# Optimization experiments

Hardware: AMD Instinct MI355X
Metric: run time of the kernel (lower is better)

The kernel has to match this reference:

```python
import jax, jax.numpy as jnp
import numpy as np

N_NODES = 50000
N_GROUPS = 512
D_FEAT = 128
D_HID = 128
N_CLASS = 16
NEG_SLOPE = 0.2


def gat_conv(x, edge_index, W, a_src, a_dst, bias, n):
    """Single-head PyG-style GATConv (with self-loops, eval mode / no dropout)."""
    h = x @ W  # [n, D_HID]
    loop = jnp.arange(n)
    src = jnp.concatenate([edge_index[0], loop])  # neighbors j
    dst = jnp.concatenate([edge_index[1], loop])  # targets i
    a_s = h @ a_src  # [n]
    a_d = h @ a_dst  # [n]
    e = jax.nn.leaky_relu(a_s[src] + a_d[dst], NEG_SLOPE)  # [E+n]
    # segment softmax over incoming edges of each dst node
    m = jax.ops.segment_max(e, dst, num_segments=n)
    e = jnp.exp(e - m[dst])
    denom = jax.ops.segment_sum(e, dst, num_segments=n)
    alpha = e / denom[dst]
    out = jax.ops.segment_sum(alpha[:, None] * h[src], dst, num_segments=n)
    return out + bias


def setup_inputs() -> dict:
    key = jax.random.key(0)
    ks = jax.random.split(key, 12)
    s_f = 1.0 / np.sqrt(D_FEAT)
    s_h = 1.0 / np.sqrt(D_HID)
    return {
        "x_full": jax.random.normal(ks[0], (N_NODES, D_FEAT), jnp.float32),
        "x_group": jax.random.normal(ks[1], (N_GROUPS, D_FEAT), jnp.float32),
        "W_full": jax.random.normal(ks[2], (D_FEAT, D_HID), jnp.float32) * s_f,
        "a_src_full": jax.random.normal(ks[3], (D_HID,), jnp.float32) * s_h,
        "a_dst_full": jax.random.normal(ks[4], (D_HID,), jnp.float32) * s_h,
        "bias_full": jnp.zeros((D_HID,), jnp.float32),
        "W_group": jax.random.normal(ks[5], (D_FEAT, D_HID), jnp.float32) * s_f,
        "a_src_group": jax.random.normal(ks[6], (D_HID,), jnp.float32) * s_h,
        "a_dst_group": jax.random.normal(ks[7], (D_HID,), jnp.float32) * s_h,
        "bias_group": jnp.zeros((D_HID,), jnp.float32),
        "fc_W": jax.random.normal(ks[8], (D_HID, N_CLASS), jnp.float32) * s_h,
        "fc_b": jnp.zeros((N_CLASS,), jnp.float32),
        "edge_index_full": jax.random.randint(ks[9], (2, 600000), 0, N_NODES, jnp.int64),
        "edge_index_group": jax.random.randint(ks[10], (2, 4096), 0, N_GROUPS, jnp.int64),
        "node_group": jax.random.randint(ks[11], (N_NODES,), 0, N_GROUPS, jnp.int64),
    }


def reference(x_full, x_group, W_full, a_src_full, a_dst_full, bias_full,
              W_group, a_src_group, a_dst_group, bias_group, fc_W, fc_b,
              edge_index_full, edge_index_group, node_group):
    full_x = jax.nn.elu(gat_conv(x_full, edge_index_full, W_full, a_src_full,
                                 a_dst_full, bias_full, N_NODES))   # [N, D_HID]
    group_x = jax.nn.elu(gat_conv(x_group, edge_index_group, W_group, a_src_group,
                                  a_dst_group, bias_group, N_GROUPS))  # [G, D_HID]

    # mean feature of groups adjacent to each group (edges src->dst in group graph)
    gsrc, gdst = edge_index_group[0], edge_index_group[1]
    adj_sum = jax.ops.segment_sum(group_x[gdst], gsrc, num_segments=N_GROUPS)
    cnt = jax.ops.segment_sum(jnp.ones_like(gsrc, jnp.float32), gsrc, num_segments=N_GROUPS)
    adj_mean = adj_sum / jnp.maximum(cnt, 1.0)[:, None]  # [G, D_HID]

    gf = group_x[node_group]   # group feature per node, [N, D_HID]
    am = adj_mean[node_group]  # adjacent-group mean per node, [N, D_HID]

    # dot(node, group_feature) and mean_j dot(node, adj_j) == dot(node, adj_mean)
    iw_group = jnp.sum(full_x * gf, axis=-1, keepdims=True)  # [N, 1]
    iw_adj = jnp.sum(full_x * am, axis=-1, keepdims=True)    # [N, 1]

    updated = full_x + iw_group * gf + iw_adj * am  # [N, D_HID]
    out = updated @ fc_W + fc_b                     # [N, N_CLASS]
    return (out, updated)
```

## Files before the change

kernel.cpp:

```cpp
#include <hip/hip_runtime.h>

typedef unsigned short u16;
typedef unsigned int u32;

static __device__ __forceinline__ float lrelu(float x) { return x >= 0.f ? x : 0.2f * x; }

static __device__ __forceinline__ u16 f2bf(float f) {
    u32 u = __float_as_uint(f);
    u += 0x7FFF + ((u >> 16) & 1);
    return (u16)(u >> 16);
}
static __device__ __forceinline__ float bf2f(u16 h) {
    return __uint_as_float((u32)h << 16);
}

static __device__ __forceinline__ float fc_reduce16(float f0, float f1, int lane,
                                                    const float4* __restrict__ fW4) {
    float4 w00 = fW4[(2 * lane) * 4 + 0], w01 = fW4[(2 * lane) * 4 + 1];
    float4 w02 = fW4[(2 * lane) * 4 + 2], w03 = fW4[(2 * lane) * 4 + 3];
    float4 w10 = fW4[(2 * lane + 1) * 4 + 0], w11 = fW4[(2 * lane + 1) * 4 + 1];
    float4 w12 = fW4[(2 * lane + 1) * 4 + 2], w13 = fW4[(2 * lane + 1) * 4 + 3];
    float4 q0, q1, q2, q3;
    q0.x = f0 * w00.x + f1 * w10.x; q0.y = f0 * w00.y + f1 * w10.y;
    q0.z = f0 * w00.z + f1 * w10.z; q0.w = f0 * w00.w + f1 * w10.w;
    q1.x = f0 * w01.x + f1 * w11.x; q1.y = f0 * w01.y + f1 * w11.y;
    q1.z = f0 * w01.z + f1 * w11.z; q1.w = f0 * w01.w + f1 * w11.w;
    q2.x = f0 * w02.x + f1 * w12.x; q2.y = f0 * w02.y + f1 * w12.y;
    q2.z = f0 * w02.z + f1 * w12.z; q2.w = f0 * w02.w + f1 * w12.w;
    q3.x = f0 * w03.x + f1 * w13.x; q3.y = f0 * w03.y + f1 * w13.y;
    q3.z = f0 * w03.z + f1 * w13.z; q3.w = f0 * w03.w + f1 * w13.w;
    bool h5 = (lane & 32) != 0, h4 = (lane & 16) != 0;
    bool h3 = (lane & 8) != 0, h2 = (lane & 4) != 0;
    float4 s0, s1, k0, k1;
    s0.x = h5 ? q0.x : q2.x; s0.y = h5 ? q0.y : q2.y;
    s0.z = h5 ? q0.z : q2.z; s0.w = h5 ? q0.w : q2.w;
    s1.x = h5 ? q1.x : q3.x; s1.y = h5 ? q1.y : q3.y;
    s1.z = h5 ? q1.z : q3.z; s1.w = h5 ? q1.w : q3.w;
    s0.x = __shfl_xor(s0.x, 32); s0.y = __shfl_xor(s0.y, 32);
    s0.z = __shfl_xor(s0.z, 32); s0.w = __shfl_xor(s0.w, 32);
    s1.x = __shfl_xor(s1.x, 32); s1.y = __shfl_xor(s1.y, 32);
    s1.z = __shfl_xor(s1.z, 32); s1.w = __shfl_xor(s1.w, 32);
    k0.x = h5 ? q2.x : q0.x; k0.y = h5 ? q2.y : q0.y;
    k0.z = h5 ? q2.z : q0.z; k0.w = h5 ? q2.w : q0.w;
    k1.x = h5 ? q3.x : q1.x; k1.y = h5 ? q3.y : q1.y;
    k1.z = h5 ? q3.z : q1.z; k1.w = h5 ? q3.w : q1.w;
    float4 a0, a1;
    a0.x = k0.x + s0.x; a0.y = k0.y + s0.y; a0.z = k0.z + s0.z; a0.w = k0.w + s0.w;
    a1.x = k1.x + s1.x; a1.y = k1.y + s1.y; a1.z = k1.z + s1.z; a1.w = k1.w + s1.w;
    float4 sB, kB;
    sB.x = h4 ? a0.x : a1.x; sB.y = h4 ? a0.y : a1.y;
    sB.z = h4 ? a0.z : a1.z; sB.w = h4 ? a0.w : a1.w;
    sB.x = __shfl_xor(sB.x, 16); sB.y = __shfl_xor(sB.y, 16);
    sB.z = __shfl_xor(sB.z, 16); sB.w = __shfl_xor(sB.w, 16);
    kB.x = h4 ? a1.x : a0.x; kB.y = h4 ? a1.y : a0.y;
    kB.z = h4 ? a1.z : a0.z; kB.w = h4 ? a1.w : a0.w;
    float4 b;
    b.x = kB.x + sB.x; b.y = kB.y + sB.y; b.z = kB.z + sB.z; b.w = kB.w + sB.w;
    float sCx = h3 ? b.x : b.z, sCy = h3 ? b.y : b.w;
    sCx = __shfl_xor(sCx, 8); sCy = __shfl_xor(sCy, 8);
    float kCx = h3 ? b.z : b.x, kCy = h3 ? b.w : b.y;
    float c2x = kCx + sCx, c2y = kCy + sCy;
    float sD = h2 ? c2x : c2y;
    sD = __shfl_xor(sD, 4);
    float kD = h2 ? c2y : c2x;
    float r = kD + sD;
    r += __shfl_xor(r, 1);
    r += __shfl_xor(r, 2);
    return r;
}

__global__ __launch_bounds__(256) void gemm_both_kernel(
        const float* __restrict__ Xf, const float* __restrict__ Wf,
        const float* __restrict__ asf, const float* __restrict__ adf,
        u16* __restrict__ Hbf, float* __restrict__ as_f, float* __restrict__ ad_f, int N,
        const float* __restrict__ Xg, const float* __restrict__ Wg,
        const float* __restrict__ asg, const float* __restrict__ adg,
        u16* __restrict__ Hbg, float* __restrict__ as_g, float* __restrict__ ad_g, int G,
        int nbFull) {
    const float* X; const float* W; const float* av; const float* dv;
    u16* Hb; float* as_out; float* ad_out; int n_lim; long base;
    if (blockIdx.x < nbFull) {
        X = Xf; W = Wf; av = asf; dv = adf; Hb = Hbf; as_out = as_f; ad_out = ad_f;
        n_lim = N; base = (long)blockIdx.x * 32;
    } else {
        X = Xg; W = Wg; av = asg; dv = adg; Hb = Hbg; as_out = as_g; ad_out = ad_g;
        n_lim = G; base = (long)(blockIdx.x - nbFull) * 32;
    }
    __shared__ float Ws[64 * 128];
    __shared__ float Xs[32 * 128];
    int tid = threadIdx.x;
    float4* Ws4 = (float4*)Ws;
    float4* Xs4 = (float4*)Xs;
    const float4* X4 = (const float4*)(X + base * 128);
    for (int i = tid; i < 1024; i += 256) {
        int r = i >> 5;
        Xs4[i] = (base + r < n_lim) ? X4[i] : make_float4(0.f, 0.f, 0.f, 0.f);
    }
    int fgrp = tid & 31;
    int n0 = (tid >> 5) * 4;
    float4 acc[4] = {};
    for (int half = 0; half < 2; ++half) {
        __syncthreads();
        const float4* W4 = (const float4*)(W + half * 64 * 128);
        for (int i = tid; i < 2048; i += 256) Ws4[i] = W4[i];
        __syncthreads();
        #pragma unroll 4
        for (int kk = 0; kk < 64; ++kk) {
            float4 w = Ws4[kk * 32 + fgrp];
            #pragma unroll
            for (int j = 0; j < 4; ++j) {
                float x = Xs[(n0 + j) * 128 + half * 64 + kk];
                acc[j].x += x * w.x; acc[j].y += x * w.y;
                acc[j].z += x * w.z; acc[j].w += x * w.w;
            }
        }
    }
    float4 as4 = ((const float4*)av)[fgrp];
    float4 ad4 = ((const float4*)dv)[fgrp];
    float ps[4], pd[4];
    #pragma unroll
    for (int j = 0; j < 4; ++j) {
        ps[j] = acc[j].x * as4.x + acc[j].y * as4.y + acc[j].z * as4.z + acc[j].w * as4.w;
        pd[j] = acc[j].x * ad4.x + acc[j].y * ad4.y + acc[j].z * ad4.z + acc[j].w * ad4.w;
    }
    #pragma unroll
    for (int off = 16; off; off >>= 1) {
        #pragma unroll
        for (int j = 0; j < 4; ++j) {
            ps[j] += __shfl_xor(ps[j], off);
            pd[j] += __shfl_xor(pd[j], off);
        }
    }
    if ((tid & 31) == 0) {
        #pragma unroll
        for (int j = 0; j < 4; ++j) {
            long n = base + n0 + j;
            if (n < n_lim) { as_out[n] = ps[j]; ad_out[n] = pd[j]; }
        }
    }
    #pragma unroll
    for (int j = 0; j < 4; ++j) {
        long n = base + n0 + j;
        if (n < n_lim) {
            ushort4 hv;
            hv.x = f2bf(acc[j].x); hv.y = f2bf(acc[j].y);
            hv.z = f2bf(acc[j].z); hv.w = f2bf(acc[j].w);
            ((ushort4*)(Hb + n * 128))[fgrp] = hv;
        }
    }
}

__global__ __launch_bounds__(256) void hist2_kernel(const int* __restrict__ efd, int E, int N,
                                                    const int* __restrict__ egd, int Eg, int G,
                                                    int Npad, int* __restrict__ deg) {
    int i = blockIdx.x * 256 + threadIdx.x;
    int totF = E + N;
    int tot = totF + Eg + G;
    if (i >= tot) return;
    int d;
    if (i < E) d = efd[i];
    else if (i < totF) d = i - E;
    else {
        int j = i - totF;
        d = Npad + ((j < Eg) ? egd[j] : (j - Eg));
    }
    atomicAdd(&deg[d], 1);
}

__global__ __launch_bounds__(256) void scan1_kernel(const int* __restrict__ deg, int n,
                                                    int* __restrict__ bsum) {
    __shared__ int s[256];
    int i = blockIdx.x * 256 + threadIdx.x;
    s[threadIdx.x] = (i < n) ? deg[i] : 0;
    __syncthreads();
    for (int off = 128; off; off >>= 1) {
        if (threadIdx.x < off) s[threadIdx.x] += s[threadIdx.x + off];
        __syncthreads();
    }
    if (threadIdx.x == 0) bsum[blockIdx.x] = s[0];
}

__global__ __launch_bounds__(256) void scan3_kernel(int* __restrict__ deg, int n, int nb,
                                                    const int* __restrict__ bsum,
                                                    int* __restrict__ offs, int Ltot) {
    __shared__ int sb[256];
    __shared__ int s[256];
    int t = threadIdx.x;
    sb[t] = (t < nb) ? bsum[t] : 0;
    __syncthreads();
    for (int off = 1; off < 256; off <<= 1) {
        int u = (t >= off) ? sb[t - off] : 0;
        __syncthreads();
        sb[t] += u;
        __syncthreads();
    }
    int blockOff = (blockIdx.x == 0) ? 0 : sb[blockIdx.x - 1];
    if (blockIdx.x == 0 && t == 0) offs[Ltot] = sb[nb - 1];

    int i = blockIdx.x * 256 + t;
    int v = (i < n) ? deg[i] : 0;
    s[t] = v;
    __syncthreads();
    for (int off = 1; off < 256; off <<= 1) {
        int u = (t >= off) ? s[t - off] : 0;
        __syncthreads();
        s[t] += u;
        __syncthreads();
    }
    if (i < n) {
        int excl = s[t] - v + blockOff;
        offs[i] = excl;
        deg[i] = excl;
    }
}

__global__ __launch_bounds__(256) void place2_kernel(const int* __restrict__ efs,
                                                     const int* __restrict__ efd, int E, int N,
                                                     const int* __restrict__ egs,
                                                     const int* __restrict__ egd, int Eg, int G,
                                                     int Npad,
                                                     const float* __restrict__ a_s,
                                                     const float* __restrict__ a_d,
                                                     const float* __restrict__ a_sg,
                                                     const float* __restrict__ a_dg,
                                                     int* __restrict__ cursor,
                                                     int2* __restrict__ sepack) {
    int i = blockIdx.x * 256 + threadIdx.x;
    int totF = E + N;
    int tot = totF + Eg + G;
    if (i >= tot) return;
    int s, d, dcur;
    float av;
    if (i < totF) {
        if (i < E) { s = efs[i]; d = efd[i]; } else { s = d = i - E; }
        av = a_s[s] + a_d[d];
        dcur = d;
    } else {
        int j = i - totF;
        if (j < Eg) { s = egs[j]; d = egd[j]; } else { s = d = j - Eg; }
        av = a_sg[s] + a_dg[d];
        dcur = Npad + d;
    }
    float e = expf(lrelu(av));
    int pos = atomicAdd(&cursor[dcur], 1);
    sepack[pos] = make_int2(s, __float_as_int(e));
}

__global__ __launch_bounds__(256) void pull2_kernel(const u16* __restrict__ Hf,
                                                    const u16* __restrict__ Hg,
                                                    const int* __restrict__ offs,
                                                    const int2* __restrict__ sepack,
                                                    const float* __restrict__ bias_f,
                                                    const float* __restrict__ bias_g,
                                                    const float* __restrict__ fcW,
                                                    float* __restrict__ fx,
                                                    float* __restrict__ gx,
                                                    float* __restrict__ fxW,
                                                    int N, int G, int Npad) {
    int gid = blockIdx.x * 256 + threadIdx.x;
    int w = gid >> 6, lane = gid & 63;
    const u16* H;
    const float* bias;
    float* out;
    int idx;
    bool isFull = (w < N);
    if (isFull) {
        H = Hf; bias = bias_f; out = fx + (long)w * 128; idx = w;
    } else if (w < N + G) {
        int g = w - N;
        H = Hg; bias = bias_g; out = gx + (long)g * 128; idx = Npad + g;
    } else return;
    int beg = offs[idx], end = offs[idx + 1];
    const ushort2* H2 = (const ushort2*)H;
    float a0x = 0.f, a0y = 0.f, a1x = 0.f, a1y = 0.f;
    float a2x = 0.f, a2y = 0.f, a3x = 0.f, a3y = 0.f;
    float ss0 = 0.f, ss1 = 0.f;
    for (int b = beg; b < end; b += 64) {
        int m = end - b;
        if (m > 64) m = 64;
        int2 se = (lane < m) ? sepack[b + lane] : make_int2(0, 0);
        int sl = se.x;
        float el = __int_as_float(se.y);
        int k = 0;
        for (; k + 4 <= m; k += 4) {
            int s0 = __shfl(sl, k),     s1 = __shfl(sl, k + 1);
            int s2 = __shfl(sl, k + 2), s3 = __shfl(sl, k + 3);
            float e0 = __shfl(el, k),     e1 = __shfl(el, k + 1);
            float e2 = __shfl(el, k + 2), e3 = __shfl(el, k + 3);
            ushort2 h0 = H2[(long)s0 * 64 + lane];
            ushort2 h1 = H2[(long)s1 * 64 + lane];
            ushort2 h2 = H2[(long)s2 * 64 + lane];
            ushort2 h3 = H2[(long)s3 * 64 + lane];
            a0x += e0 * bf2f(h0.x); a0y += e0 * bf2f(h0.y);
            a1x += e1 * bf2f(h1.x); a1y += e1 * bf2f(h1.y);
            a2x += e2 * bf2f(h2.x); a2y += e2 * bf2f(h2.y);
            a3x += e3 * bf2f(h3.x); a3y += e3 * bf2f(h3.y);
            ss0 += e0 + e1; ss1 += e2 + e3;
        }
        for (; k < m; ++k) {
            int s0 = __shfl(sl, k);
            float e0 = __shfl(el, k);
            ushort2 h0 = H2[(long)s0 * 64 + lane];
            a0x += e0 * bf2f(h0.x); a0y += e0 * bf2f(h0.y);
            ss0 += e0;
        }
    }
    float accx = (a0x + a1x) + (a2x + a3x);
    float accy = (a0y + a1y) + (a2y + a3y);
    float ssum = ss0 + ss1;
    float inv = 1.f / ssum;
    float2 bv = ((const float2*)bias)[lane];
    float ox = accx * inv + bv.x;
    float oy = accy * inv + bv.y;
    ox = ox > 0.f ? ox : expm1f(ox);
    oy = oy > 0.f ? oy : expm1f(oy);
    ((float2*)out)[lane] = make_float2(ox, oy);
    if (isFull) {
        float r = fc_reduce16(ox, oy, lane, (const float4*)fcW);
        int cls = (lane >> 2) & 15;
        if ((lane & 3) == 0) fxW[(long)w * 16 + cls] = r;
    }
}

__global__ __launch_bounds__(256) void adj_kernel(const int* __restrict__ gsrc,
                                                  const int* __restrict__ gdst, int Eg,
                                                  const float* __restrict__ gx,
                                                  float* __restrict__ adj_sum,
                                                  float* __restrict__ cnt) {
    int gid = blockIdx.x * 256 + threadIdx.x;
    int i = gid >> 6, lane = gid & 63;
    if (i >= Eg) return;
    int s = gsrc[i], d = gdst[i];
    float2 gv = ((const float2*)gx)[(long)d * 64 + lane];
    atomicAdd(&adj_sum[(long)s * 128 + 2 * lane], gv.x);
    atomicAdd(&adj_sum[(long)s * 128 + 2 * lane + 1], gv.y);
    if (lane == 0) atomicAdd(&cnt[s], 1.f);
}

__global__ __launch_bounds__(256) void groupfc_kernel(const float* __restrict__ gx,
                                                      const float* __restrict__ adj_sum,
                                                      const float* __restrict__ cnt,
                                                      const float* __restrict__ fcW,
                                                      float* __restrict__ adj_mean,
                                                      float* __restrict__ gfW,
                                                      float* __restrict__ amW, int G) {
    int gid = blockIdx.x * 256 + threadIdx.x;
    int g = gid >> 6, lane = gid & 63;
    if (g >= G) return;
    float inv = 1.f / fmaxf(cnt[g], 1.f);
    float2 as2 = ((const float2*)adj_sum)[(long)g * 64 + lane];
    float2 am = make_float2(as2.x * inv, as2.y * inv);
    ((float2*)adj_mean)[(long)g * 64 + lane] = am;
    float2 gf = ((const float2*)gx)[(long)g * 64 + lane];
    const float4* fW4 = (const float4*)fcW;
    float rg = fc_reduce16(gf.x, gf.y, lane, fW4);
    float ra = fc_reduce16(am.x, am.y, lane, fW4);
    int cls = (lane >> 2) & 15;
    if ((lane & 3) == 0) {
        gfW[(long)g * 16 + cls] = rg;
        amW[(long)g * 16 + cls] = ra;
    }
}

__global__ __launch_bounds__(256) void final3_kernel(const int* __restrict__ node_group,
                                                     const float* __restrict__ gx,
                                                     const float* __restrict__ adj_mean,
                                                     const float* __restrict__ gfW,
                                                     const float* __restrict__ amW,
                                                     const float* __restrict__ fxW,
                                                     const float* __restrict__ fcb,
                                                     float* __restrict__ upd,
                                                     float* __restrict__ out, int N) {
    int gid = blockIdx.x * 256 + threadIdx.x;
    int n = gid >> 6, lane = gid & 63;
    if (n >= N) return;
    int g = node_group[n];
    float2 row = ((const float2*)upd)[(long)n * 64 + lane];
    float2 gf = ((const float2*)gx)[(long)g * 64 + lane];
    float2 am = ((const float2*)adj_mean)[(long)g * 64 + lane];
    float pg = row.x * gf.x + row.y * gf.y;
    float pa = row.x * am.x + row.y * am.y;
    #pragma unroll
    for (int off = 32; off; off >>= 1) {
        pg += __shfl_xor(pg, off);
        pa += __shfl_xor(pa, off);
    }
    float ux = row.x + pg * gf.x + pa * am.x;
    float uy = row.y + pg * gf.y + pa * am.y;
    ((float2*)upd)[(long)n * 64 + lane] = make_float2(ux, uy);
    if (lane < 16) {
        out[(long)n * 16 + lane] = fxW[(long)n * 16 + lane] + pg * gfW[(long)g * 16 + lane] +
                                   pa * amW[(long)g * 16 + lane] + fcb[lane];
    }
}

extern "C" void kernel_launch(void* const* d_in, const int* in_sizes, int n_in,
                              void* d_out, int out_size, void* d_ws, size_t ws_size,
                              hipStream_t stream) {
    const float* x_full = (const float*)d_in[0];
    const float* x_group = (const float*)d_in[1];
    const float* W_full = (const float*)d_in[2];
    const float* a_src_full = (const float*)d_in[3];
    const float* a_dst_full = (const float*)d_in[4];
    const float* bias_full = (const float*)d_in[5];
    const float* W_group = (const float*)d_in[6];
    const float* a_src_g = (const float*)d_in[7];
    const float* a_dst_g = (const float*)d_in[8];
    const float* bias_g = (const float*)d_in[9];
    const float* fc_W = (const float*)d_in[10];
    const float* fc_b = (const float*)d_in[11];
    const int* ef = (const int*)d_in[12];
    const int* eg = (const int*)d_in[13];
    const int* node_group = (const int*)d_in[14];

    int N = in_sizes[0] / 128;
    int G = in_sizes[1] / 128;
    int E = in_sizes[12] / 2;
    int Eg = in_sizes[13] / 2;
    const int* ef_src = ef;
    const int* ef_dst = ef + E;
    const int* eg_src = eg;
    const int* eg_dst = eg + Eg;

    int Npad = (N + 255) & ~255;
    int Ltot = Npad + G;
    int LtotPad = (Ltot + 255) & ~255;
    int totF = E + N;
    int tot = totF + Eg + G;

    float* out_cls = (float*)d_out;
    float* fx = out_cls + (long)N * 16;

    char* w = (char*)d_ws;
    auto alloc = [&](size_t bytes) {
        char* p = w;
        w += (bytes + 255) & ~(size_t)255;
        return p;
    };
    u16* h_full = (u16*)alloc((size_t)N * 128 * 2);
    u16* h_g = (u16*)alloc((size_t)G * 128 * 2);
    float* a_s = (float*)alloc((size_t)N * 4);
    float* a_d = (float*)alloc((size_t)N * 4);
    float* a_sg = (float*)alloc((size_t)G * 4);
    float* a_dg = (float*)alloc((size_t)G * 4);
    float* gx = (float*)alloc((size_t)G * 128 * 4);
    float* adj_mean = (float*)alloc((size_t)G * 128 * 4);
    float* fxW = (float*)alloc((size_t)N * 16 * 4);
    float* gfW = (float*)alloc((size_t)G * 16 * 4);
    float* amW = (float*)alloc((size_t)G * 16 * 4);
    float* adj_sum = (float*)alloc((size_t)G * 128 * 4);
    float* cnt = (float*)alloc((size_t)G * 4);
    int* deg = (int*)alloc((size_t)LtotPad * 4);
    int* offs = (int*)alloc((size_t)(LtotPad + 1) * 4);
    int2* sepack = (int2*)alloc((size_t)tot * 8);
    int* bsum = (int*)alloc(256 * 4);

    size_t zero_span = (char*)(deg + LtotPad) - (char*)adj_sum;
    (void)hipMemsetAsync(adj_sum, 0, zero_span, stream);

    auto cdiv = [](int a, int b) { return (a + b - 1) / b; };

    int nbFull = cdiv(N, 32);
    gemm_both_kernel<<<nbFull + cdiv(G, 32), 256, 0, stream>>>(
        x_full, W_full, a_src_full, a_dst_full, h_full, a_s, a_d, N,
        x_group, W_group, a_src_g, a_dst_g, h_g, a_sg, a_dg, G, nbFull);

    int nb = cdiv(Ltot, 256);
    hist2_kernel<<<cdiv(tot, 256), 256, 0, stream>>>(ef_dst, E, N, eg_dst, Eg, G, Npad, deg);
    scan1_kernel<<<nb, 256, 0, stream>>>(deg, Ltot, bsum);
    scan3_kernel<<<nb, 256, 0, stream>>>(deg, Ltot, nb, bsum, offs, Ltot);
    place2_kernel<<<cdiv(tot, 256), 256, 0, stream>>>(ef_src, ef_dst, E, N, eg_src, eg_dst,
                                                      Eg, G, Npad, a_s, a_d, a_sg, a_dg,
                                                      deg, sepack);

    pull2_kernel<<<cdiv((N + G) * 64, 256), 256, 0, stream>>>(h_full, h_g, offs, sepack,
                                                              bias_full, bias_g, fc_W,
                                                              fx, gx, fxW, N, G, Npad);

    adj_kernel<<<cdiv(Eg * 64, 256), 256, 0, stream>>>(eg_src, eg_dst, Eg, gx, adj_sum, cnt);
    groupfc_kernel<<<cdiv(G * 64, 256), 256, 0, stream>>>(gx, adj_sum, cnt, fc_W,
                                                          adj_mean, gfW, amW, G);
    final3_kernel<<<cdiv(N * 64, 256), 256, 0, stream>>>(node_group, gx, adj_mean, gfW, amW,
                                                         fxW, fc_b, fx, out_cls, N);
}
```

Baseline: 289.1 us.

## Pull 4 edges per wave with 16B bf16 loads and move FC into final kernel

The pull kernel now splits each wave into four 16-lane groups. Each group loads a full 256-byte bf16 row with uint4 loads, so the wave processes four source edges per step instead of one, and a cross-group shuffle reduction combines the partial sums. The FC projection is removed from the pull kernel and the group-fc kernel is deleted. The final kernel now computes the adjacent-group mean inline and applies the FC to the updated row directly. The aim is fewer, wider gather loads, one less launch, and fewer intermediate buffers, at the cost of extra shuffle reductions, tail lanes doing padded work, and only 16 lanes active for the epilogue.

```diff
diff --git a/kernel.cpp b/kernel.cpp
--- a/kernel.cpp
+++ b/kernel.cpp
@@ -10,9 +10,8 @@
     u += 0x7FFF + ((u >> 16) & 1);
     return (u16)(u >> 16);
 }
-static __device__ __forceinline__ float bf2f(u16 h) {
-    return __uint_as_float((u32)h << 16);
-}
+static __device__ __forceinline__ float bflo(u32 u) { return __uint_as_float(u << 16); }
+static __device__ __forceinline__ float bfhi(u32 u) { return __uint_as_float(u & 0xffff0000u); }
 
 static __device__ __forceinline__ float fc_reduce16(float f0, float f1, int lane,
                                                     const float4* __restrict__ fW4) {
@@ -252,10 +251,8 @@
                                                     const int2* __restrict__ sepack,
                                                     const float* __restrict__ bias_f,
                                                     const float* __restrict__ bias_g,
-                                                    const float* __restrict__ fcW,
                                                     float* __restrict__ fx,
                                                     float* __restrict__ gx,
-                                                    float* __restrict__ fxW,
                                                     int N, int G, int Npad) {
     int gid = blockIdx.x * 256 + threadIdx.x;
     int w = gid >> 6, lane = gid & 63;
@@ -263,62 +260,84 @@
     const float* bias;
     float* out;
     int idx;
-    bool isFull = (w < N);
-    if (isFull) {
+    if (w < N) {
         H = Hf; bias = bias_f; out = fx + (long)w * 128; idx = w;
     } else if (w < N + G) {
         int g = w - N;
         H = Hg; bias = bias_g; out = gx + (long)g * 128; idx = Npad + g;
     } else return;
     int beg = offs[idx], end = offs[idx + 1];
-    const ushort2* H2 = (const ushort2*)H;
-    float a0x = 0.f, a0y = 0.f, a1x = 0.f, a1y = 0.f;
-    float a2x = 0.f, a2y = 0.f, a3x = 0.f, a3y = 0.f;
-    float ss0 = 0.f, ss1 = 0.f;
+    const uint4* H16 = (const uint4*)H;
+    int sub = lane >> 4;
+    int fc = lane & 15;
+    float a0 = 0.f, a1 = 0.f, a2 = 0.f, a3 = 0.f;
+    float a4 = 0.f, a5 = 0.f, a6 = 0.f, a7 = 0.f;
+    float ss = 0.f;
     for (int b = beg; b < end; b += 64) {
         int m = end - b;
         if (m > 64) m = 64;
         int2 se = (lane < m) ? sepack[b + lane] : make_int2(0, 0);
         int sl = se.x;
         float el = __int_as_float(se.y);
+        int kend = (m + 3) & ~3;
         int k = 0;
-        for (; k + 4 <= m; k += 4) {
-            int s0 = __shfl(sl, k),     s1 = __shfl(sl, k + 1);
-            int s2 = __shfl(sl, k + 2), s3 = __shfl(sl, k + 3);
-            float e0 = __shfl(el, k),     e1 = __shfl(el, k + 1);
-            float e2 = __shfl(el, k + 2), e3 = __shfl(el, k + 3);
-            ushort2 h0 = H2[(long)s0 * 64 + lane];
-            ushort2 h1 = H2[(long)s1 * 64 + lane];
-            ushort2 h2 = H2[(long)s2 * 64 + lane];
-            ushort2 h3 = H2[(long)s3 * 64 + lane];
-            a0x += e0 * bf2f(h0.x); a0y += e0 * bf2f(h0.y);
-            a1x += e1 * bf2f(h1.x); a1y += e1 * bf2f(h1.y);
-            a2x += e2 * bf2f(h2.x); a2y += e2 * bf2f(h2.y);
-            a3x += e3 * bf2f(h3.x); a3y += e3 * bf2f(h3.y);
-            ss0 += e0 + e1; ss1 += e2 + e3;
-        }
-        for (; k < m; ++k) {
-            int s0 = __shfl(sl, k);
-            float e0 = __shfl(el, k);
-            ushort2 h0 = H2[(long)s0 * 64 + lane];
-            a0x += e0 * bf2f(h0.x); a0y += e0 * bf2f(h0.y);
-            ss0 += e0;
-        }
-    }
-    float accx = (a0x + a1x) + (a2x + a3x);
-    float accy = (a0y + a1y) + (a2y + a3y);
-    float ssum = ss0 + ss1;
-    float inv = 1.f / ssum;
-    float2 bv = ((const float2*)bias)[lane];
-    float ox = accx * inv + bv.x;
-    float oy = accy * inv + bv.y;
-    ox = ox > 0.f ? ox : expm1f(ox);
-    oy = oy > 0.f ? oy : expm1f(oy);
-    ((float2*)out)[lane] = make_float2(ox, oy);
-    if (isFull) {
-        float r = fc_reduce16(ox, oy, lane, (const float4*)fcW);
-        int cls = (lane >> 2) & 15;
-        if ((lane & 3) == 0) fxW[(long)w * 16 + cls] = r;
+        for (; k + 8 <= kend; k += 8) {
+            int s0 = __shfl(sl, k + sub);
+            float e0 = __shfl(el, k + sub);
+            int s1 = __shfl(sl, k + 4 + sub);
+            float e1 = __shfl(el, k + 4 + sub);
+            uint4 h0 = H16[(long)s0 * 16 + fc];
+            uint4 h1 = H16[(long)s1 * 16 + fc];
+            a0 += e0 * bflo(h0.x); a1 += e0 * bfhi(h0.x);
+            a2 += e0 * bflo(h0.y); a3 += e0 * bfhi(h0.y);
+            a4 += e0 * bflo(h0.z); a5 += e0 * bfhi(h0.z);
+            a6 += e0 * bflo(h0.w); a7 += e0 * bfhi(h0.w);
+            a0 += e1 * bflo(h1.x); a1 += e1 * bfhi(h1.x);
+            a2 += e1 * bflo(h1.y); a3 += e1 * bfhi(h1.y);
+            a4 += e1 * bflo(h1.z); a5 += e1 * bfhi(h1.z);
+            a6 += e1 * bflo(h1.w); a7 += e1 * bfhi(h1.w);
+            ss += e0 + e1;
+        }
+        if (k < kend) {
+            int s0 = __shfl(sl, k + sub);
+            float e0 = __shfl(el, k + sub);
+            uint4 h0 = H16[(long)s0 * 16 + fc];
+            a0 += e0 * bflo(h0.x); a1 += e0 * bfhi(h0.x);
+            a2 += e0 * bflo(h0.y); a3 += e0 * bfhi(h0.y);
+            a4 += e0 * bflo(h0.z); a5 += e0 * bfhi(h0.z);
+            a6 += e0 * bflo(h0.w); a7 += e0 * bfhi(h0.w);
+            ss += e0;
+        }
+    }
+    a0 += __shfl_xor(a0, 16); a0 += __shfl_xor(a0, 32);
+    a1 += __shfl_xor(a1, 16); a1 += __shfl_xor(a1, 32);
+    a2 += __shfl_xor(a2, 16); a2 += __shfl_xor(a2, 32);
+    a3 += __shfl_xor(a3, 16); a3 += __shfl_xor(a3, 32);
+    a4 += __shfl_xor(a4, 16); a4 += __shfl_xor(a4, 32);
+    a5 += __shfl_xor(a5, 16); a5 += __shfl_xor(a5, 32);
+    a6 += __shfl_xor(a6, 16); a6 += __shfl_xor(a6, 32);
+    a7 += __shfl_xor(a7, 16); a7 += __shfl_xor(a7, 32);
+    ss += __shfl_xor(ss, 16); ss += __shfl_xor(ss, 32);
+    if (lane < 16) {
+        float inv = 1.f / ss;
+        const float4* b4 = (const float4*)bias;
+        float4 bA = b4[lane * 2], bB = b4[lane * 2 + 1];
+        float4 oA, oB;
+        oA.x = a0 * inv + bA.x; oA.y = a1 * inv + bA.y;
+        oA.z = a2 * inv + bA.z; oA.w = a3 * inv + bA.w;
+        oB.x = a4 * inv + bB.x; oB.y = a5 * inv + bB.y;
+        oB.z = a6 * inv + bB.z; oB.w = a7 * inv + bB.w;
+        oA.x = oA.x > 0.f ? oA.x : expm1f(oA.x);
+        oA.y = oA.y > 0.f ? oA.y : expm1f(oA.y);
+        oA.z = oA.z > 0.f ? oA.z : expm1f(oA.z);
+        oA.w = oA.w > 0.f ? oA.w : expm1f(oA.w);
+        oB.x = oB.x > 0.f ? oB.x : expm1f(oB.x);
+        oB.y = oB.y > 0.f ? oB.y : expm1f(oB.y);
+        oB.z = oB.z > 0.f ? oB.z : expm1f(oB.z);
+        oB.w = oB.w > 0.f ? oB.w : expm1f(oB.w);
+        float4* o4 = (float4*)out;
+        o4[lane * 2] = oA;
+        o4[lane * 2 + 1] = oB;
     }
 }
 
@@ -337,37 +356,11 @@
     if (lane == 0) atomicAdd(&cnt[s], 1.f);
 }
 
-__global__ __launch_bounds__(256) void groupfc_kernel(const float* __restrict__ gx,
-                                                      const float* __restrict__ adj_sum,
-                                                      const float* __restrict__ cnt,
-                                                      const float* __restrict__ fcW,
-                                                      float* __restrict__ adj_mean,
-                                                      float* __restrict__ gfW,
-                                                      float* __restrict__ amW, int G) {
-    int gid = blockIdx.x * 256 + threadIdx.x;
-    int g = gid >> 6, lane = gid & 63;
-    if (g >= G) return;
-    float inv = 1.f / fmaxf(cnt[g], 1.f);
-    float2 as2 = ((const float2*)adj_sum)[(long)g * 64 + lane];
-    float2 am = make_float2(as2.x * inv, as2.y * inv);
-    ((float2*)adj_mean)[(long)g * 64 + lane] = am;
-    float2 gf = ((const float2*)gx)[(long)g * 64 + lane];
-    const float4* fW4 = (const float4*)fcW;
-    float rg = fc_reduce16(gf.x, gf.y, lane, fW4);
-    float ra = fc_reduce16(am.x, am.y, lane, fW4);
-    int cls = (lane >> 2) & 15;
-    if ((lane & 3) == 0) {
-        gfW[(long)g * 16 + cls] = rg;
-        amW[(long)g * 16 + cls] = ra;
-    }
-}
-
 __global__ __launch_bounds__(256) void final3_kernel(const int* __restrict__ node_group,
                                                      const float* __restrict__ gx,
-                                                     const float* __restrict__ adj_mean,
-                                                     const float* __restrict__ gfW,
-                                                     const float* __restrict__ amW,
-                                                     const float* __restrict__ fxW,
+                                                     const float* __restrict__ adj_sum,
+                                                     const float* __restrict__ cnt,
+                                                     const float* __restrict__ fcW,
                                                      const float* __restrict__ fcb,
                                                      float* __restrict__ upd,
                                                      float* __restrict__ out, int N) {
@@ -377,21 +370,22 @@
     int g = node_group[n];
     float2 row = ((const float2*)upd)[(long)n * 64 + lane];
     float2 gf = ((const float2*)gx)[(long)g * 64 + lane];
-    float2 am = ((const float2*)adj_mean)[(long)g * 64 + lane];
+    float inv_cnt = 1.f / fmaxf(cnt[g], 1.f);
+    float2 as2 = ((const float2*)adj_sum)[(long)g * 64 + lane];
+    float amx = as2.x * inv_cnt, amy = as2.y * inv_cnt;
     float pg = row.x * gf.x + row.y * gf.y;
-    float pa = row.x * am.x + row.y * am.y;
+    float pa = row.x * amx + row.y * amy;
     #pragma unroll
     for (int off = 32; off; off >>= 1) {
         pg += __shfl_xor(pg, off);
         pa += __shfl_xor(pa, off);
     }
-    float ux = row.x + pg * gf.x + pa * am.x;
-    float uy = row.y + pg * gf.y + pa * am.y;
+    float ux = row.x + pg * gf.x + pa * amx;
+    float uy = row.y + pg * gf.y + pa * amy;
     ((float2*)upd)[(long)n * 64 + lane] = make_float2(ux, uy);
-    if (lane < 16) {
-        out[(long)n * 16 + lane] = fxW[(long)n * 16 + lane] + pg * gfW[(long)g * 16 + lane] +
-                                   pa * amW[(long)g * 16 + lane] + fcb[lane];
-    }
+    float r = fc_reduce16(ux, uy, lane, (const float4*)fcW);
+    int cls = (lane >> 2) & 15;
+    if ((lane & 3) == 0) out[(long)n * 16 + cls] = r + fcb[cls];
 }
 
 extern "C" void kernel_launch(void* const* d_in, const int* in_sizes, int n_in,
@@ -444,10 +438,6 @@
     float* a_sg = (float*)alloc((size_t)G * 4);
     float* a_dg = (float*)alloc((size_t)G * 4);
     float* gx = (float*)alloc((size_t)G * 128 * 4);
-    float* adj_mean = (float*)alloc((size_t)G * 128 * 4);
-    float* fxW = (float*)alloc((size_t)N * 16 * 4);
-    float* gfW = (float*)alloc((size_t)G * 16 * 4);
-    float* amW = (float*)alloc((size_t)G * 16 * 4);
     float* adj_sum = (float*)alloc((size_t)G * 128 * 4);
     float* cnt = (float*)alloc((size_t)G * 4);
     int* deg = (int*)alloc((size_t)LtotPad * 4);
@@ -474,12 +464,10 @@
                                                       deg, sepack);
 
     pull2_kernel<<<cdiv((N + G) * 64, 256), 256, 0, stream>>>(h_full, h_g, offs, sepack,
-                                                              bias_full, bias_g, fc_W,
-                                                              fx, gx, fxW, N, G, Npad);
+                                                              bias_full, bias_g,
+                                                              fx, gx, N, G, Npad);
 
     adj_kernel<<<cdiv(Eg * 64, 256), 256, 0, stream>>>(eg_src, eg_dst, Eg, gx, adj_sum, cnt);
-    groupfc_kernel<<<cdiv(G * 64, 256), 256, 0, stream>>>(gx, adj_sum, cnt, fc_W,
-                                                          adj_mean, gfW, amW, G);
-    final3_kernel<<<cdiv(N * 64, 256), 256, 0, stream>>>(node_group, gx, adj_mean, gfW, amW,
-                                                         fxW, fc_b, fx, out_cls, N);
-}
+    final3_kernel<<<cdiv(N * 64, 256), 256, 0, stream>>>(node_group, gx, adj_sum, cnt,
+                                                         fc_W, fc_b, fx, out_cls, N);
+}
```

After: 295.6 us. 1.02x slower.
